# Optimization experiments

Hardware: AMD Instinct MI355X
Metric: run time of the kernel (lower is better)

## Reference

```python
import jax, jax.numpy as jnp
import numpy as np

# ---- hyperparameters (from args defaults) ----
TEMPERATURE = 0.07
ALPHA = 0.5
OT_EPSILON = 0.1
OT_ITERS = 20
HOLO_WEIGHT = 1.0
RKD_DISTANCE_WEIGHT = 1.0
RKD_ANGLE_WEIGHT = 2.0
GLOBAL_RKD_WEIGHT = 10.0
MATRYOSHKA_DIMS = [128, 768]
MATRYOSHKA_WEIGHTS = [1.0, 2.0]

B, N, H_S, H_T, D_REP = 64, 256, 768, 1024, 768


def l2norm(x, axis=-1):
    # F.normalize(p=2): x / max(||x||, eps)
    n = jnp.sqrt(jnp.sum(x * x, axis=axis, keepdims=True))
    return x / jnp.maximum(n, 1e-12)


def pairwise_distance(x):
    # [n, d] -> [n, n] squared-euclidean-style distances
    sq = jnp.sum(x * x, axis=1, keepdims=True)
    return sq + sq.T - 2.0 * (x @ x.T)


def huber(diff):
    a = jnp.abs(diff)
    return jnp.where(a < 1.0, 0.5 * a * a, a - 0.5)


def rkd_distance_loss(s, t):
    n = s.shape[0]
    mask = jnp.triu(jnp.ones((n, n), dtype=bool), k=1)
    cnt = jnp.sum(mask.astype(s.dtype))
    ds, dt = pairwise_distance(s), pairwise_distance(t)
    mean_s = jax.lax.stop_gradient(jnp.sum(jnp.where(mask, ds, 0.0)) / cnt) + 1e-8
    mean_t = jax.lax.stop_gradient(jnp.sum(jnp.where(mask, dt, 0.0)) / cnt) + 1e-8
    loss = huber(ds / mean_s - dt / mean_t)
    return jnp.sum(jnp.where(mask, loss, 0.0)) / cnt


def angle_potentials(x):
    # diffs[i, j] = x[j] - x[i]
    diffs = x[None, :, :] - x[:, None, :]
    e = diffs / (jnp.linalg.norm(diffs, axis=-1, keepdims=True) + 1e-8)
    return jnp.einsum('ijd,kjd->ijk', e, e)


def rkd_angle_loss(s, t):
    psi_s, psi_t = angle_potentials(s), angle_potentials(t)
    n = psi_s.shape[0]
    idx = jnp.arange(n)
    i, j, k = idx[:, None, None], idx[None, :, None], idx[None, None, :]
    mask = (i != j) & (i != k) & (j != k)  # exclude degenerate triplets
    cnt = jnp.sum(mask.astype(s.dtype))
    loss = huber(psi_s - psi_t)
    return jnp.sum(jnp.where(mask, loss, 0.0)) / cnt


def saliency_measure(h, temp=1.0):
    # softmax over token axis of hidden-state norms -> [B, N, 1]
    norms = jnp.linalg.norm(h, axis=-1)
    return jax.nn.softmax(norms / temp, axis=-1)[..., None]


def structure_matrix(z):
    zn = l2norm(z, axis=-1)
    return 1.0 - jnp.einsum('bnd,bmd->bnm', zn, zn)


def sinkhorn_knopp_log_domain(C, mu, nu):
    # C: [B, Ns, Nt]; mu: [B, Ns, 1]; nu: [B, Nt, 1]
    log_K = -C / OT_EPSILON
    log_mu = jnp.log(mu + 1e-8)
    log_nu = jnp.log(nu + 1e-8)
    u = jnp.zeros_like(mu)
    v = jnp.zeros_like(nu)
    for _ in range(OT_ITERS):
        u = log_mu - jax.scipy.special.logsumexp(
            log_K + jnp.swapaxes(v, 1, 2), axis=2, keepdims=True)
        v = log_nu - jax.scipy.special.logsumexp(
            jnp.swapaxes(log_K, 1, 2) + jnp.swapaxes(u, 1, 2),
            axis=2, keepdims=True)
    return jnp.exp(u + log_K + jnp.swapaxes(v, 1, 2))


def fused_gromov_wasserstein(z_s, z_t, proj_w, proj_b):
    mu = saliency_measure(z_s)   # [B, N, 1]
    nu = saliency_measure(z_t)   # [B, N, 1]
    C_s = structure_matrix(z_s)  # [B, N, N]
    C_t = structure_matrix(z_t)
    z_s_norm = l2norm(z_s @ proj_w + proj_b, axis=-1)
    z_t_norm = l2norm(z_t, axis=-1)
    M = 1.0 - jnp.einsum('bnd,bmd->bnm', z_s_norm, z_t_norm)
    Gamma = sinkhorn_knopp_log_domain(M, mu, nu)
    feat_loss = jnp.mean(jnp.sum(M * Gamma, axis=(1, 2)))
    Gamma_norm = Gamma / (jnp.sum(Gamma, axis=2, keepdims=True) + 1e-8)
    C_t_mapped = jnp.einsum('bnm,bmk,blk->bnl', Gamma_norm, C_t, Gamma_norm)
    w = jnp.einsum('bni,bmi->bnm', mu, mu)  # mu @ mu^T
    struct_loss = jnp.mean(jnp.sum((C_s - C_t_mapped) ** 2 * w, axis=(1, 2)))
    return (1.0 - ALPHA) * feat_loss + ALPHA * struct_loss


def cross_entropy_inbatch(scores):
    # labels = arange(B)
    logZ = jax.scipy.special.logsumexp(scores, axis=1)
    return jnp.mean(logZ - jnp.diagonal(scores))


def setup_inputs() -> dict:
    key = jax.random.key(0)
    ks = jax.random.split(key, 10)
    return {
        's_q_reps': jax.random.normal(ks[0], (B, D_REP), jnp.float32),
        's_p_reps': jax.random.normal(ks[1], (B, D_REP), jnp.float32),
        't_q_reps': jax.random.normal(ks[2], (B, D_REP), jnp.float32),
        't_p_reps': jax.random.normal(ks[3], (B, D_REP), jnp.float32),
        's_q_states': jax.random.normal(ks[4], (B, N, H_S), jnp.float32),
        's_p_states': jax.random.normal(ks[5], (B, N, H_S), jnp.float32),
        't_q_states': jax.random.normal(ks[6], (B, N, H_T), jnp.float32),
        't_p_states': jax.random.normal(ks[7], (B, N, H_T), jnp.float32),
        'proj_w': jax.random.normal(ks[8], (H_S, H_T), jnp.float32) * (H_S ** -0.5),
        'proj_b': jnp.zeros((H_T,), jnp.float32),
    }


def reference(s_q_reps, s_p_reps, t_q_reps, t_p_reps,
              s_q_states, s_p_states, t_q_states, t_p_states,
              proj_w, proj_b):
    # teacher outputs are computed under torch.no_grad()
    t_q_reps = jax.lax.stop_gradient(t_q_reps)
    t_p_reps = jax.lax.stop_gradient(t_p_reps)
    t_q_states = jax.lax.stop_gradient(t_q_states)
    t_p_states = jax.lax.stop_gradient(t_p_states)

    contrastive_acc = 0.0
    holo_acc = 0.0
    rkd_acc = 0.0
    for dim, dim_weight in zip(MATRYOSHKA_DIMS, MATRYOSHKA_WEIGHTS):
        s_q_slice = l2norm(s_q_reps[:, :dim])
        s_p_slice = l2norm(s_p_reps[:, :dim])
        scores = (s_q_slice @ s_p_slice.T) / TEMPERATURE
        contrastive_acc += dim_weight * cross_entropy_inbatch(scores)
        if dim <= 128:
            s_batch = jnp.concatenate([s_q_slice, s_p_slice], axis=0)
            t_batch = jnp.concatenate(
                [l2norm(t_q_reps[:, :dim]), l2norm(t_p_reps[:, :dim])], axis=0)
            loss_dist = rkd_distance_loss(s_batch, t_batch)
            loss_angle = rkd_angle_loss(s_batch, t_batch)
            rkd_val = (RKD_DISTANCE_WEIGHT * loss_dist
                       + RKD_ANGLE_WEIGHT * loss_angle)
            rkd_acc += GLOBAL_RKD_WEIGHT * rkd_val * 2.0
        else:
            loss_q = fused_gromov_wasserstein(s_q_states, t_q_states, proj_w, proj_b)
            loss_p = fused_gromov_wasserstein(s_p_states, t_p_states, proj_w, proj_b)
            holo_acc += HOLO_WEIGHT * 0.5 * (loss_q + loss_p)
    return contrastive_acc + holo_acc + rkd_acc
```

## Files before the change

### kernel.cpp

```cpp
#include <hip/hip_runtime.h>
#include <math.h>

#define NB   64
#define NN   256
#define HSS  768
#define HTT  1024
#define ROWS (NB*NN)
#define C2LOG 14.426950408889634f

typedef unsigned short u16;
typedef __attribute__((ext_vector_type(8))) short bf16x8;
typedef __attribute__((ext_vector_type(4))) float f32x4;

#define LIDX(r,c) (((r)<<8) + (((((c)>>3) + (r)) & 31)<<3) + ((c)&7))
#define EIDX(r,c) (((r)<<7) + (((((c)>>3) + (r)) & 15)<<3) + ((c)&7))

__device__ __forceinline__ void gl16(const u16* g, u16* l){
  __builtin_amdgcn_global_load_lds(
      (const __attribute__((address_space(1))) unsigned int*)g,
      (__attribute__((address_space(3))) unsigned int*)l,
      16, 0, 0);
}

static const size_t OFF_ACC   = 0;
static const size_t OFF_SQ128 = 16;
static const size_t OFF_SP128 = OFF_SQ128 + 64*128;
static const size_t OFF_TQ128 = OFF_SP128 + 64*128;
static const size_t OFF_TP128 = OFF_TQ128 + 64*128;
static const size_t OFF_SQ768 = OFF_TP128 + 64*128;
static const size_t OFF_SP768 = OFF_SQ768 + 64*768;
static const size_t OFF_DS    = OFF_SP768 + 64*768;
static const size_t OFF_DT    = OFF_DS + 128*128;
static const size_t OFF_CS    = OFF_DT + 128*128;
static const size_t OFF_MBF   = OFF_CS  + (size_t)2*NB*NN*NN;
static const size_t OFF_ZS_BF = OFF_MBF + (size_t)NB*NN*NN;
static const size_t OFF_ZT_BF = OFF_ZS_BF + (size_t)ROWS*HSS/2;
static const size_t OFF_WT_BF = OFF_ZT_BF + (size_t)ROWS*HTT/2;
static const size_t OFF_ZSP_BF= OFF_WT_BF + (size_t)HTT*HSS/2;
static const size_t OFF_GN_BF = OFF_ZSP_BF+ (size_t)ROWS*HTT/2;
static const size_t OFF_CT_BF = OFF_GN_BF + (size_t)NB*NN*NN;
static const size_t OFF_T_BF  = OFF_ZS_BF;
static const size_t OFF_NS    = OFF_CT_BF + (size_t)NB*NN*NN;
static const size_t OFF_NT    = OFF_NS + ROWS;
static const size_t OFF_NSP   = OFF_NT + ROWS;
static const size_t OFF_MU    = OFF_NSP + ROWS;
static const size_t OFF_NU    = OFF_MU + 2*ROWS;


__device__ __forceinline__ float wred_sum(float v){
  #pragma unroll
  for(int o=32;o>0;o>>=1) v += __shfl_xor(v,o,64);
  return v;
}
__device__ __forceinline__ float wred_max(float v){
  #pragma unroll
  for(int o=32;o>0;o>>=1) v = fmaxf(v, __shfl_xor(v,o,64));
  return v;
}
__device__ __forceinline__ u16 f2bf(float f){
  unsigned u = __float_as_uint(f);
  unsigned r = (u + 0x7fffu + ((u>>16)&1u)) >> 16;
  return (u16)r;
}
__device__ __forceinline__ float bf2f(u16 h){
  return __uint_as_float(((unsigned)h)<<16);
}
__device__ __forceinline__ float rdlane(float v, int srcLane){
  return __uint_as_float(__builtin_amdgcn_readlane(__float_as_uint(v), srcLane));
}

__global__ __launch_bounds__(256) void k_l2norm_all(
    const float* __restrict__ sq, const float* __restrict__ sp,
    const float* __restrict__ tq, const float* __restrict__ tp,
    float* __restrict__ ws){
  int bid = blockIdx.x;
  int r = bid & 63;
  const float* in; float* out; int kuse;
  if(bid < 64)       { in = sq; out = ws + OFF_SQ128; kuse = 128; }
  else if(bid < 128) { in = sp; out = ws + OFF_SP128; kuse = 128; }
  else if(bid < 192) { in = tq; out = ws + OFF_TQ128; kuse = 128; }
  else if(bid < 256) { in = tp; out = ws + OFF_TP128; kuse = 128; }
  else if(bid < 320) { in = sq; out = ws + OFF_SQ768; kuse = 768; }
  else               { in = sp; out = ws + OFF_SP768; kuse = 768; }
  const float* row = in + (size_t)r*768;
  float ss = 0.f;
  for(int d=threadIdx.x; d<kuse; d+=256){ float x=row[d]; ss += x*x; }
  ss = wred_sum(ss);
  __shared__ float sm[4];
  if((threadIdx.x&63)==0) sm[threadIdx.x>>6]=ss;
  __syncthreads();
  float tot = sm[0]+sm[1]+sm[2]+sm[3];
  float inv = 1.f / fmaxf(sqrtf(tot), 1e-12f);
  for(int d=threadIdx.x; d<kuse; d+=256) out[(size_t)r*kuse + d] = row[d]*inv;
}

__global__ __launch_bounds__(512) void k_contrastive2(const float* __restrict__ ws,
    float* __restrict__ acc){
  int bid = blockIdx.x;
  int i = bid & 63;
  int big = bid >> 6;
  const float* q = ws + (big ? OFF_SQ768 : OFF_SQ128);
  const float* p = ws + (big ? OFF_SP768 : OFF_SP128);
  int dim = big ? 768 : 128;
  float weight = big ? 2.f : 1.f;
  int j = threadIdx.x & 63;
  int part = threadIdx.x >> 6;
  const float* qi = q + (size_t)i*dim;
  const float* pj = p + (size_t)j*dim;
  int seg = dim >> 3;
  int d0 = part*seg;
  float dot = 0.f;
  for(int d=d0; d<d0+seg; d+=4){
    float4 a = *(const float4*)(qi+d);
    float4 b = *(const float4*)(pj+d);
    dot = fmaf(a.x,b.x,dot);
    dot = fmaf(a.y,b.y,dot);
    dot = fmaf(a.z,b.z,dot);
    dot = fmaf(a.w,b.w,dot);
  }
  __shared__ float sm[8][64];
  sm[part][j] = dot;
  __syncthreads();
  if(part==0){
    float s = 0.f;
    #pragma unroll
    for(int k=0;k<8;k++) s += sm[k][j];
    s = s / 0.07f;
    float mx = wred_max(s);
    float e = expf(s - mx);
    float Z = wred_sum(e);
    float logZ = mx + logf(Z);
    float diag = __shfl(s, i, 64);
    if(j==0) atomicAdd(acc+0, weight*(logZ - diag)*(1.f/64.f));
  }
}

__global__ __launch_bounds__(128) void k_gram_ds(const float* __restrict__ sb,
    const float* __restrict__ tb, float* __restrict__ ds, float* __restrict__ dt,
    float* __restrict__ acc){
  int r = blockIdx.x, c = threadIdx.x;
  const float* sr = sb + r*128; const float* sc = sb + c*128;
  const float* tr = tb + r*128; const float* tc = tb + c*128;
  float dot_s=0,ssr=0,ssc=0,dot_t=0,tsr=0,tsc=0;
  for(int d=0; d<128; d++){
    float a=sr[d], b=sc[d]; dot_s += a*b; ssr += a*a; ssc += b*b;
    float at=tr[d], bt=tc[d]; dot_t += at*bt; tsr += at*at; tsc += bt*bt;
  }
  float dv = ssr + ssc - 2.f*dot_s;
  float tv = tsr + tsc - 2.f*dot_t;
  ds[r*128+c] = dv; dt[r*128+c] = tv;
  float ms = (c>r)? dv : 0.f;
  float mt = (c>r)? tv : 0.f;
  ms = wred_sum(ms); mt = wred_sum(mt);
  __shared__ float sm[2][2];
  if((threadIdx.x&63)==0){ sm[0][threadIdx.x>>6]=ms; sm[1][threadIdx.x>>6]=mt; }
  __syncthreads();
  if(threadIdx.x==0){ atomicAdd(acc+1, sm[0][0]+sm[0][1]); atomicAdd(acc+2, sm[1][0]+sm[1][1]); }
}

__global__ __launch_bounds__(128) void k_rkd_dist(const float* __restrict__ ds,
    const float* __restrict__ dt, float* __restrict__ acc){
  int r=blockIdx.x, c=threadIdx.x;
  float mean_s = acc[1]*(1.f/8128.f) + 1e-8f;
  float mean_t = acc[2]*(1.f/8128.f) + 1e-8f;
  float h=0.f;
  if(c>r){
    float diff = ds[r*128+c]/mean_s - dt[r*128+c]/mean_t;
    float a = fabsf(diff);
    h = (a<1.f)? 0.5f*a*a : a-0.5f;
  }
  h = wred_sum(h);
  __shared__ float sm[2];
  if((threadIdx.x&63)==0) sm[threadIdx.x>>6]=h;
  __syncthreads();
  if(threadIdx.x==0) atomicAdd(acc+3, sm[0]+sm[1]);
}

#define RKD_LDS 65536
__global__ __launch_bounds__(256, 1) void k_rkd_angle_mfma(
    const float* __restrict__ sb, const float* __restrict__ tb,
    float* __restrict__ accp)
{
  extern __shared__ u16 eSh[];
  u16* Es = eSh;
  u16* Et = eSh + 128*128;
  const int j    = blockIdx.x >> 1;
  const int half = blockIdx.x & 1;
  const int tid = threadIdx.x;
  {
    const int i = tid >> 1, h = tid & 1;
    #pragma unroll
    for(int which=0; which<2; which++){
      const float* xb = which ? tb : sb;
      u16* E = which ? Et : Es;
      const float* xj = xb + j*128 + h*64;
      const float* xi = xb + i*128 + h*64;
      float ss = 0.f;
      #pragma unroll
      for(int d4=0; d4<16; d4++){
        float4 a = *(const float4*)(xj + d4*4);
        float4 b = *(const float4*)(xi + d4*4);
        float d0=a.x-b.x, d1=a.y-b.y, d2=a.z-b.z, d3=a.w-b.w;
        ss += d0*d0+d1*d1+d2*d2+d3*d3;
      }
      ss += __shfl_xor(ss, 1, 64);
      float inv = (i==j) ? 0.f : 1.f/(sqrtf(ss)+1e-8f);
      #pragma unroll
      for(int d4=0; d4<16; d4++){
        float4 a = *(const float4*)(xj + d4*4);
        float4 b = *(const float4*)(xi + d4*4);
        int c = h*64 + d4*4;
        E[EIDX(i,c+0)] = f2bf((a.x-b.x)*inv);
        E[EIDX(i,c+1)] = f2bf((a.y-b.y)*inv);
        E[EIDX(i,c+2)] = f2bf((a.z-b.z)*inv);
        E[EIDX(i,c+3)] = f2bf((a.w-b.w)*inv);
      }
    }
  }
  __syncthreads();
  const int w = tid >> 6, lane = tid & 63;
  const int q = lane >> 4, loc = lane & 15;
  float hsum = 0.f;
  #pragma unroll
  for(int ni=0; ni<4; ni++){
    const int cb = half*64 + ni*16;
    #pragma unroll
    for(int mi=0; mi<2; mi++){
      const int rb = w*32 + mi*16;
      f32x4 as_ = {0.f,0.f,0.f,0.f}, at_ = {0.f,0.f,0.f,0.f};
      #pragma unroll
      for(int k0=0; k0<128; k0+=32){
        int ra = rb + loc, rbn = cb + loc;
        int ca = k0 + q*8;
        bf16x8 aS = *(const bf16x8*)(Es + EIDX(ra, ca));
        bf16x8 bS = *(const bf16x8*)(Es + EIDX(rbn, ca));
        bf16x8 aT = *(const bf16x8*)(Et + EIDX(ra, ca));
        bf16x8 bT = *(const bf16x8*)(Et + EIDX(rbn, ca));
        as_ = __builtin_amdgcn_mfma_f32_16x16x32_bf16(aS, bS, as_, 0,0,0);
        at_ = __builtin_amdgcn_mfma_f32_16x16x32_bf16(aT, bT, at_, 0,0,0);
      }
      #pragma unroll
      for(int jj=0; jj<4; jj++){
        int row = rb + q*4 + jj, col = cb + loc;
        if(row != col){
          float d = as_[jj] - at_[jj];
          float a = fabsf(d);
          hsum += (a < 1.f) ? 0.5f*a*a : a - 0.5f;
        }
      }
    }
  }
  hsum = wred_sum(hsum);
  __syncthreads();
  float* red = (float*)eSh;
  if(lane==0) red[w] = hsum;
  __syncthreads();
  if(tid==0) atomicAdd(accp+4, red[0]+red[1]+red[2]+red[3]);
}

__global__ __launch_bounds__(256) void k_cvt_norm(const float* __restrict__ in,
    u16* __restrict__ out, float* __restrict__ nrm, int K){
  int w = threadIdx.x >> 6, l = threadIdx.x & 63;
  int r = blockIdx.x*4 + w;
  const float* row = in + (size_t)r*K;
  u16* orow = out + (size_t)r*K;
  float ss = 0.f;
  int nv = K >> 8;
  for(int i=0;i<nv;i++){
    int d = l*4 + i*256;
    float4 x = *(const float4*)(row + d);
    ushort4 o; o.x=f2bf(x.x); o.y=f2bf(x.y); o.z=f2bf(x.z); o.w=f2bf(x.w);
    *(ushort4*)(orow + d) = o;
    ss += x.x*x.x + x.y*x.y + x.z*x.z + x.w*x.w;
  }
  ss = wred_sum(ss);
  if(l==0) nrm[r] = sqrtf(ss);
}

__global__ __launch_bounds__(256) void k_row_norm_bf16(const u16* __restrict__ z,
    float* __restrict__ nrm, int K){
  int w = threadIdx.x >> 6, l = threadIdx.x & 63;
  int r = blockIdx.x*4 + w;
  const u16* row = z + (size_t)r*K;
  float ss = 0.f;
  int nv = K >> 9;
  for(int i=0;i<nv;i++){
    int d = l*8 + i*512;
    uint4 v = *(const uint4*)(row + d);
    float a0=__uint_as_float(v.x<<16), a1=__uint_as_float(v.x&0xffff0000u);
    float a2=__uint_as_float(v.y<<16), a3=__uint_as_float(v.y&0xffff0000u);
    float a4=__uint_as_float(v.z<<16), a5=__uint_as_float(v.z&0xffff0000u);
    float a6=__uint_as_float(v.w<<16), a7=__uint_as_float(v.w&0xffff0000u);
    ss += a0*a0+a1*a1+a2*a2+a3*a3+a4*a4+a5*a5+a6*a6+a7*a7;
  }
  ss = wred_sum(ss);
  if(l==0) nrm[r] = sqrtf(ss);
}

__global__ void k_wt(const float* __restrict__ W, u16* __restrict__ Wt){
  __shared__ float t[32][33];
  int k0 = blockIdx.y*32, n0 = blockIdx.x*32;
  int tx = threadIdx.x, ty = threadIdx.y;
  for(int r=0;r<32;r+=8) t[ty+r][tx] = W[(size_t)(k0+ty+r)*HTT + n0+tx];
  __syncthreads();
  for(int r=0;r<32;r+=8) Wt[(size_t)(n0+ty+r)*HSS + k0+tx] = f2bf(t[tx][ty+r]);
}

__global__ __launch_bounds__(256) void k_saliency2(const float* __restrict__ ns,
    const float* __restrict__ nt, float* __restrict__ omu, float* __restrict__ onu){
  int b0 = blockIdx.x, n = threadIdx.x;
  const float* nrm = (b0 < NB) ? ns : nt;
  float* out = (b0 < NB) ? omu : onu;
  int b = b0 & 63;
  float x = nrm[b*NN+n];
  float mx = wred_max(x);
  __shared__ float sm[4], sm2[4];
  if((n&63)==0) sm[n>>6]=mx;
  __syncthreads();
  mx = fmaxf(fmaxf(sm[0],sm[1]),fmaxf(sm[2],sm[3]));
  float e = expf(x-mx);
  float s = wred_sum(e);
  if((n&63)==0) sm2[n>>6]=s;
  __syncthreads();
  s = sm2[0]+sm2[1]+sm2[2]+sm2[3];
  out[b*NN+n] = e/s;
}

enum { MODE_PROJ=0, MODE_COST=1, MODE_PLAIN=2, MODE_STRUCT=3 };

template<int MODE>
__global__ __launch_bounds__(256) void k_mfma(
    const u16* __restrict__ A, int lda, long bA,
    const u16* __restrict__ B, int ldb, long bB,
    int K,
    float* __restrict__ outF, u16* __restrict__ outB, int ldo, long bO,
    const float* __restrict__ nx, const float* __restrict__ ny,
    const float* __restrict__ bias,
    const float* __restrict__ Cs, const float* __restrict__ mu,
    float* __restrict__ accp)
{
  __shared__ u16 As[128*32];
  __shared__ u16 Bs[128*32];
  __shared__ float red[4];

  int gx = gridDim.x, gy = gridDim.y;
  int flat = blockIdx.x + gx*(blockIdx.y + gy*blockIdx.z);
  int nwg  = gx*gy*gridDim.z;
  int cpx  = nwg >> 3;
  int lg   = (flat & 7)*cpx + (flat >> 3);
  int bx   = lg % gx;
  int rest = lg / gx;
  int by   = rest % gy;
  int b    = rest / gy;

  const u16* Ab = A + (size_t)b*bA;
  const u16* Bb = B + (size_t)b*bB;
  int tid = threadIdx.x;
  int lane = tid & 63, w = tid >> 6;
  int m0 = by*128, n0 = bx*128;
  int row_off = (w>>1)*64, col_off = (w&1)*64;
  int q = lane>>4, loc = lane&15;
  f32x4 acc[4][4] = {};

  const int srow = (lane >> 2);
  const int sslot = lane & 3;

  for(int k0=0;k0<K;k0+=32){
    #pragma unroll
    for(int h=0;h<2;h++){
      int row = h*64 + w*16 + srow;
      int ca  = (sslot ^ ((row>>1)&3))*8;
      u16* ldst = As + h*2048 + w*512 + lane*8;
      u16* ldstB= Bs + h*2048 + w*512 + lane*8;
      gl16(Ab + (size_t)(m0+row)*lda + k0 + ca, ldst);
      gl16(Bb + (size_t)(n0+row)*ldb + k0 + ca, ldstB);
    }
    __syncthreads();
    bf16x8 af[4], bfr[4];
    #pragma unroll
    for(int mi=0;mi<4;mi++){
      int r = row_off + mi*16 + loc;
      int slot = q ^ ((r>>1)&3);
      af[mi] = *(const bf16x8*)(As + r*32 + slot*8);
    }
    #pragma unroll
    for(int ni=0;ni<4;ni++){
      int r = col_off + ni*16 + loc;
      int slot = q ^ ((r>>1)&3);
      bfr[ni] = *(const bf16x8*)(Bs + r*32 + slot*8);
    }
    #pragma unroll
    for(int mi=0;mi<4;mi++)
      #pragma unroll
      for(int ni=0;ni<4;ni++)
        acc[mi][ni] = __builtin_amdgcn_mfma_f32_16x16x32_bf16(af[mi], bfr[ni], acc[mi][ni], 0,0,0);
    __syncthreads();
  }

  float* outFb = outF ? outF + (size_t)b*bO : nullptr;
  u16*   outBb = outB ? outB + (size_t)b*bO : nullptr;
  const float* nxb = nx ? nx + (size_t)b*NN : nullptr;
  const float* nyb = ny ? ny + (size_t)b*NN : nullptr;
  const float* Cb  = (MODE==MODE_STRUCT) ? Cs + (size_t)b*bO : nullptr;
  const float* mb  = (MODE==MODE_STRUCT) ? mu + (size_t)b*NN : nullptr;
  float lsum = 0.f;
  #pragma unroll
  for(int mi=0;mi<4;mi++){
    #pragma unroll
    for(int j=0;j<4;j++){
      int row = m0 + row_off + mi*16 + q*4 + j;
      float ir = 0.f, mr = 0.f;
      if(MODE==MODE_COST)   ir = 1.f/fmaxf(nxb[row],1e-12f);
      if(MODE==MODE_STRUCT) mr = mb[row];
      #pragma unroll
      for(int ni=0;ni<4;ni++){
        int col = n0 + col_off + ni*16 + loc;
        float v = acc[mi][ni][j];
        if(MODE==MODE_PROJ){
          v += bias[col];
          outBb[(size_t)row*ldo + col] = f2bf(v);
        } else if(MODE==MODE_COST){
          float ic = 1.f/fmaxf(nyb[col],1e-12f);
          v = 1.f - v*ir*ic;
          if(outFb) outFb[(size_t)row*ldo + col] = v;
          if(outBb) outBb[(size_t)row*ldo + col] = f2bf(v);
        } else if(MODE==MODE_PLAIN){
          outBb[(size_t)row*ldo + col] = f2bf(v);
        } else {
          float d = Cb[(size_t)row*ldo + col] - v;
          lsum += d*d*mr*mb[col];
        }
      }
    }
  }
  if(MODE==MODE_STRUCT){
    lsum = wred_sum(lsum);
    if(lane==0) red[w] = lsum;
    __syncthreads();
    if(tid==0) atomicAdd(accp+6, red[0]+red[1]+red[2]+red[3]);
  }
}

#define SINK_DYN_LDS 131072
__global__ __launch_bounds__(1024, 1) void k_sinkhorn_fused(
    const u16* __restrict__ Mbf, const float* __restrict__ muL,
    const float* __restrict__ nuL, u16* __restrict__ Gn, float* __restrict__ accp)
{
  extern __shared__ u16 Ks[];
  __shared__ __align__(16) float partA[1024];
  __shared__ __align__(16) float partB[4096];
  __shared__ __align__(16) float svw[1024];
  __shared__ __align__(16) float smu_s[256], snu_s[256], sv_ep[256];
  __shared__ float red[16];

  const int b = blockIdx.x;
  const int t = threadIdx.x;
  const u16* Mb = Mbf + (size_t)b*NN*NN;

  #pragma unroll
  for(int i=0;i<16;i++){
    int e = (i*1024 + t)*4;
    int r = e>>8, c = e&255;
    ushort4 mv = *(const ushort4*)(Mb + e);
    ushort4 o;
    o.x = f2bf(exp2f(-C2LOG*bf2f(mv.x)));
    o.y = f2bf(exp2f(-C2LOG*bf2f(mv.y)));
    o.z = f2bf(exp2f(-C2LOG*bf2f(mv.z)));
    o.w = f2bf(exp2f(-C2LOG*bf2f(mv.w)));
    *(ushort4*)(Ks + LIDX(r,c)) = o;
  }
  if(t < NN){
    smu_s[t] = muL[(size_t)b*NN+t] + 1e-8f;
    snu_s[t] = nuL[(size_t)b*NN+t] + 1e-8f;
  }
  __syncthreads();

  const int w = t>>6, l = t&63;
  const int r_ = t & 255, p_ = t >> 8;
  const int rw = (w<<4) + (l&15);
  const int cl = (p_<<6) + l;
  float* svslot = svw + (w<<6);

  uint4 kreg[8];
  #pragma unroll
  for(int jj=0;jj<8;jj++)
    kreg[jj] = *(const uint4*)(Ks + LIDX(r_, (p_<<6)+(jj<<3)));

  #pragma unroll 1
  for(int it=0; it<21; it++){
    float vl;
    if(it==0){ vl = 1.f; }
    else {
      float t0=0.f,t1=0.f,t2=0.f,t3=0.f;
      #pragma unroll
      for(int ww=0; ww<4; ww++){
        t0 += partB[((ww*4+0)<<8) + cl];
        t1 += partB[((ww*4+1)<<8) + cl];
        t2 += partB[((ww*4+2)<<8) + cl];
        t3 += partB[((ww*4+3)<<8) + cl];
      }
      vl = snu_s[cl] / ((t0+t1)+(t2+t3));
    }
    svslot[l] = vl;
    if(it==20 && (w&3)==0) sv_ep[cl] = vl;
    float s0=0.f, s1=0.f, s2=0.f, s3=0.f;
    #pragma unroll
    for(int jj=0;jj<8;jj++){
      uint4 kv = kreg[jj];
      float4 va = *(const float4*)(svslot + (jj<<3));
      float4 vb = *(const float4*)(svslot + (jj<<3) + 4);
      s0 = fmaf(__uint_as_float(kv.x<<16),           va.x, s0);
      s1 = fmaf(__uint_as_float(kv.x & 0xffff0000u), va.y, s1);
      s2 = fmaf(__uint_as_float(kv.y<<16),           va.z, s2);
      s3 = fmaf(__uint_as_float(kv.y & 0xffff0000u), va.w, s3);
      s0 = fmaf(__uint_as_float(kv.z<<16),           vb.x, s0);
      s1 = fmaf(__uint_as_float(kv.z & 0xffff0000u), vb.y, s1);
      s2 = fmaf(__uint_as_float(kv.w<<16),           vb.z, s2);
      s3 = fmaf(__uint_as_float(kv.w & 0xffff0000u), vb.w, s3);
    }
    float sacc = (s0+s1)+(s2+s3);
    if(it==20) svw[t] = sacc;
    else       partA[t] = sacc;
    __syncthreads();
    if(it==20) break;

    float S = (partA[rw] + partA[256+rw]) + (partA[512+rw] + partA[768+rw]);
    float ul = smu_s[rw] / S;
    float cs0=0.f,cs1=0.f,cs2=0.f,cs3=0.f;
    #pragma unroll
    for(int rr=0; rr<16; rr++){
      float ur = rdlane(ul, rr);
      ushort4 kv = *(const ushort4*)(Ks + LIDX((w<<4)+rr, l<<2));
      cs0 = fmaf(bf2f(kv.x), ur, cs0);
      cs1 = fmaf(bf2f(kv.y), ur, cs1);
      cs2 = fmaf(bf2f(kv.z), ur, cs2);
      cs3 = fmaf(bf2f(kv.w), ur, cs3);
    }
    float4 o; o.x=cs0; o.y=cs1; o.z=cs2; o.w=cs3;
    *(float4*)(partB + (w<<8) + (l<<2)) = o;
    __syncthreads();
  }

  float Sold = (partA[rw] + partA[256+rw]) + (partA[512+rw] + partA[768+rw]);
  float ul   = smu_s[rw] / Sold;
  float Snew = (svw[rw] + svw[256+rw]) + (svw[512+rw] + svw[768+rw]);
  float invl = 1.f / (ul*Snew + 1e-8f);

  u16* Gb = Gn + (size_t)b*NN*NN;
  const float IC = -1.f/C2LOG;
  float4 v4 = *(const float4*)(sv_ep + (l<<2));
  float fl = 0.f;
  #pragma unroll
  for(int rr=0; rr<16; rr++){
    int r = (w<<4) + rr;
    float ur  = rdlane(ul, rr);
    float inv = rdlane(invl, rr);
    ushort4 kv = *(const ushort4*)(Ks + LIDX(r, l<<2));
    float k0=bf2f(kv.x), k1=bf2f(kv.y), k2=bf2f(kv.z), k3=bf2f(kv.w);
    float g0=ur*k0*v4.x, g1=ur*k1*v4.y, g2=ur*k2*v4.z, g3=ur*k3*v4.w;
    fl += g0*(__log2f(k0)*IC) + g1*(__log2f(k1)*IC)
        + g2*(__log2f(k2)*IC) + g3*(__log2f(k3)*IC);
    ushort4 o;
    o.x=f2bf(g0*inv); o.y=f2bf(g1*inv); o.z=f2bf(g2*inv); o.w=f2bf(g3*inv);
    *(ushort4*)(Gb + (size_t)r*NN + (l<<2)) = o;
  }
  fl = wred_sum(fl);
  if(l==0) red[w] = fl;
  __syncthreads();
  if(t==0){
    float s=0.f;
    #pragma unroll
    for(int i=0;i<16;i++) s+=red[i];
    atomicAdd(accp+5, s);
  }
}

__global__ void k_final(const float* __restrict__ acc, float* __restrict__ out){
  out[0] = acc[0]
         + 20.f*acc[3]*(1.f/8128.f)
         + 40.f*acc[4]*(1.f/2048256.f)
         + 0.25f*(acc[5]+acc[6])*(1.f/64.f);
}

extern "C" void kernel_launch(void* const* d_in, const int* in_sizes, int n_in,
                              void* d_out, int out_size, void* d_ws, size_t ws_size,
                              hipStream_t stream) {
  const float* s_q_reps   = (const float*)d_in[0];
  const float* s_p_reps   = (const float*)d_in[1];
  const float* t_q_reps   = (const float*)d_in[2];
  const float* t_p_reps   = (const float*)d_in[3];
  const float* s_q_states = (const float*)d_in[4];
  const float* s_p_states = (const float*)d_in[5];
  const float* t_q_states = (const float*)d_in[6];
  const float* t_p_states = (const float*)d_in[7];
  const float* proj_w     = (const float*)d_in[8];
  const float* proj_b     = (const float*)d_in[9];
  float* ws = (float*)d_ws;
  float* acc = ws + OFF_ACC;
  u16* M_BF   = (u16*)(ws + OFF_MBF);
  u16* ZS_BF  = (u16*)(ws + OFF_ZS_BF);
  u16* ZT_BF  = (u16*)(ws + OFF_ZT_BF);
  u16* WT_BF  = (u16*)(ws + OFF_WT_BF);
  u16* ZSP_BF = (u16*)(ws + OFF_ZSP_BF);
  u16* GN_BF  = (u16*)(ws + OFF_GN_BF);
  u16* CT_BF  = (u16*)(ws + OFF_CT_BF);
  u16* T_BF   = (u16*)(ws + OFF_T_BF);

  hipFuncSetAttribute(reinterpret_cast<const void*>(k_sinkhorn_fused),
                      hipFuncAttributeMaxDynamicSharedMemorySize, SINK_DYN_LDS);
  hipFuncSetAttribute(reinterpret_cast<const void*>(k_rkd_angle_mfma),
                      hipFuncAttributeMaxDynamicSharedMemorySize, RKD_LDS);

  hipMemsetAsync(acc, 0, 16*sizeof(float), stream);

  k_l2norm_all<<<384,256,0,stream>>>(s_q_reps, s_p_reps, t_q_reps, t_p_reps, ws);
  k_contrastive2<<<128,512,0,stream>>>(ws, acc);
  k_gram_ds<<<128,128,0,stream>>>(ws+OFF_SQ128, ws+OFF_TQ128, ws+OFF_DS, ws+OFF_DT, acc);
  k_rkd_dist<<<128,128,0,stream>>>(ws+OFF_DS, ws+OFF_DT, acc);
  k_rkd_angle_mfma<<<256,256,RKD_LDS,stream>>>(ws+OFF_SQ128, ws+OFF_TQ128, acc);

  k_wt<<<dim3(HTT/32, HSS/32),dim3(32,8),0,stream>>>(proj_w, WT_BF);

  for(int pass=0; pass<2; pass++){
    const float* zs = pass ? s_p_states : s_q_states;
    const float* zt = pass ? t_p_states : t_q_states;
    size_t po  = (size_t)pass*NB*NN*NN;
    size_t pr  = (size_t)pass*ROWS;
    k_cvt_norm<<<ROWS/4,256,0,stream>>>(zs, ZS_BF, ws+OFF_NS, HSS);
    k_cvt_norm<<<ROWS/4,256,0,stream>>>(zt, ZT_BF, ws+OFF_NT, HTT);
    k_saliency2<<<128,256,0,stream>>>(ws+OFF_NS, ws+OFF_NT, ws+OFF_MU+pr, ws+OFF_NU+pr);
    k_mfma<MODE_PROJ><<<dim3(HTT/128, ROWS/128, 1),256,0,stream>>>(
        ZS_BF, HSS, 0, WT_BF, HSS, 0, HSS,
        nullptr, ZSP_BF, HTT, 0,
        nullptr, nullptr, proj_b, nullptr, nullptr, nullptr);
    k_row_norm_bf16<<<ROWS/4,256,0,stream>>>(ZSP_BF, ws+OFF_NSP, HTT);
    k_mfma<MODE_COST><<<dim3(2,2,NB),256,0,stream>>>(
        ZS_BF, HSS, (long)NN*HSS, ZS_BF, HSS, (long)NN*HSS, HSS,
        ws+OFF_CS+po, nullptr, NN, (long)NN*NN,
        ws+OFF_NS, ws+OFF_NS, nullptr, nullptr, nullptr, nullptr);
    k_mfma<MODE_COST><<<dim3(2,2,NB),256,0,stream>>>(
        ZT_BF, HTT, (long)NN*HTT, ZT_BF, HTT, (long)NN*HTT, HTT,
        nullptr, CT_BF+po, NN, (long)NN*NN,
        ws+OFF_NT, ws+OFF_NT, nullptr, nullptr, nullptr, nullptr);
    k_mfma<MODE_COST><<<dim3(2,2,NB),256,0,stream>>>(
        ZSP_BF, HTT, (long)NN*HTT, ZT_BF, HTT, (long)NN*HTT, HTT,
        nullptr, M_BF+po, NN, (long)NN*NN,
        ws+OFF_NSP, ws+OFF_NT, nullptr, nullptr, nullptr, nullptr);
  }

  k_sinkhorn_fused<<<2*NB,1024,SINK_DYN_LDS,stream>>>(
      M_BF, ws+OFF_MU, ws+OFF_NU, GN_BF, acc);

  k_mfma<MODE_PLAIN><<<dim3(2,2,2*NB),256,0,stream>>>(
      GN_BF, NN, (long)NN*NN, CT_BF, NN, (long)NN*NN, NN,
      nullptr, T_BF, NN, (long)NN*NN,
      nullptr, nullptr, nullptr, nullptr, nullptr, nullptr);
  k_mfma<MODE_STRUCT><<<dim3(2,2,2*NB),256,0,stream>>>(
      T_BF, NN, (long)NN*NN, GN_BF, NN, (long)NN*NN, NN,
      nullptr, nullptr, NN, (long)NN*NN,
      nullptr, nullptr, nullptr, ws+OFF_CS, ws+OFF_MU, acc);

  k_final<<<1,1,0,stream>>>(acc, (float*)d_out);
}
```

Measured before the change: 680.0 us.

## Restructure Sinkhorn loop to stream K from LDS and use shuffle reductions

The fused Sinkhorn kernel no longer caches a row slice of K in registers. Each iteration now reads K from LDS for the row-sum matvec. Row and column partial sums are reduced with wave shuffles instead of separate LDS partial buffers, and u, v and the final inverse are kept in shared arrays. The column-normalisation step becomes its own phase with an extra barrier per iteration. This cuts register pressure and LDS footprint, but adds LDS traffic for K and one more __syncthreads per iteration.

```diff
diff --git a/kernel.cpp b/kernel.cpp
--- a/kernel.cpp
+++ b/kernel.cpp
@@ -64,9 +64,6 @@
 }
 __device__ __forceinline__ float bf2f(u16 h){
   return __uint_as_float(((unsigned)h)<<16);
-}
-__device__ __forceinline__ float rdlane(float v, int srcLane){
-  return __uint_as_float(__builtin_amdgcn_readlane(__float_as_uint(v), srcLane));
 }
 
 __global__ __launch_bounds__(256) void k_l2norm_all(
@@ -447,10 +444,8 @@
     const float* __restrict__ nuL, u16* __restrict__ Gn, float* __restrict__ accp)
 {
   extern __shared__ u16 Ks[];
-  __shared__ __align__(16) float partA[1024];
   __shared__ __align__(16) float partB[4096];
-  __shared__ __align__(16) float svw[1024];
-  __shared__ __align__(16) float smu_s[256], snu_s[256], sv_ep[256];
+  __shared__ __align__(16) float su[256], sv[256], smu_s[256], snu_s[256], sinv[256];
   __shared__ float red[16];
 
   const int b = blockIdx.x;
@@ -472,43 +467,23 @@
   if(t < NN){
     smu_s[t] = muL[(size_t)b*NN+t] + 1e-8f;
     snu_s[t] = nuL[(size_t)b*NN+t] + 1e-8f;
+    sv[t] = 1.f;
   }
   __syncthreads();
 
   const int w = t>>6, l = t&63;
-  const int r_ = t & 255, p_ = t >> 8;
-  const int rw = (w<<4) + (l&15);
-  const int cl = (p_<<6) + l;
-  float* svslot = svw + (w<<6);
-
-  uint4 kreg[8];
-  #pragma unroll
-  for(int jj=0;jj<8;jj++)
-    kreg[jj] = *(const uint4*)(Ks + LIDX(r_, (p_<<6)+(jj<<3)));
+  const int ra = (w<<4) + (l&15);
+  const int qa = l>>4;
 
   #pragma unroll 1
-  for(int it=0; it<21; it++){
-    float vl;
-    if(it==0){ vl = 1.f; }
-    else {
-      float t0=0.f,t1=0.f,t2=0.f,t3=0.f;
-      #pragma unroll
-      for(int ww=0; ww<4; ww++){
-        t0 += partB[((ww*4+0)<<8) + cl];
-        t1 += partB[((ww*4+1)<<8) + cl];
-        t2 += partB[((ww*4+2)<<8) + cl];
-        t3 += partB[((ww*4+3)<<8) + cl];
-      }
-      vl = snu_s[cl] / ((t0+t1)+(t2+t3));
-    }
-    svslot[l] = vl;
-    if(it==20 && (w&3)==0) sv_ep[cl] = vl;
+  for(int it=0; it<=20; ++it){
     float s0=0.f, s1=0.f, s2=0.f, s3=0.f;
     #pragma unroll
     for(int jj=0;jj<8;jj++){
-      uint4 kv = kreg[jj];
-      float4 va = *(const float4*)(svslot + (jj<<3));
-      float4 vb = *(const float4*)(svslot + (jj<<3) + 4);
+      int c0 = (qa<<6) + (jj<<3);
+      uint4 kv = *(const uint4*)(Ks + LIDX(ra, c0));
+      float4 va = *(const float4*)(sv + c0);
+      float4 vb = *(const float4*)(sv + c0 + 4);
       s0 = fmaf(__uint_as_float(kv.x<<16),           va.x, s0);
       s1 = fmaf(__uint_as_float(kv.x & 0xffff0000u), va.y, s1);
       s2 = fmaf(__uint_as_float(kv.y<<16),           va.z, s2);
@@ -518,19 +493,22 @@
       s2 = fmaf(__uint_as_float(kv.w<<16),           vb.z, s2);
       s3 = fmaf(__uint_as_float(kv.w & 0xffff0000u), vb.w, s3);
     }
-    float sacc = (s0+s1)+(s2+s3);
-    if(it==20) svw[t] = sacc;
-    else       partA[t] = sacc;
+    float S = (s0+s1)+(s2+s3);
+    S += __shfl_xor(S, 16, 64);
+    S += __shfl_xor(S, 32, 64);
+    if(qa==0){
+      if(it<20) su[ra]   = smu_s[ra] / S;
+      else      sinv[ra] = 1.f / (su[ra]*S + 1e-8f);
+    }
     __syncthreads();
     if(it==20) break;
 
-    float S = (partA[rw] + partA[256+rw]) + (partA[512+rw] + partA[768+rw]);
-    float ul = smu_s[rw] / S;
     float cs0=0.f,cs1=0.f,cs2=0.f,cs3=0.f;
     #pragma unroll
     for(int rr=0; rr<16; rr++){
-      float ur = rdlane(ul, rr);
-      ushort4 kv = *(const ushort4*)(Ks + LIDX((w<<4)+rr, l<<2));
+      int r = (w<<4) + rr;
+      ushort4 kv = *(const ushort4*)(Ks + LIDX(r, l<<2));
+      float ur = su[r];
       cs0 = fmaf(bf2f(kv.x), ur, cs0);
       cs1 = fmaf(bf2f(kv.y), ur, cs1);
       cs2 = fmaf(bf2f(kv.z), ur, cs2);
@@ -539,22 +517,27 @@
     float4 o; o.x=cs0; o.y=cs1; o.z=cs2; o.w=cs3;
     *(float4*)(partB + (w<<8) + (l<<2)) = o;
     __syncthreads();
-  }
-
-  float Sold = (partA[rw] + partA[256+rw]) + (partA[512+rw] + partA[768+rw]);
-  float ul   = smu_s[rw] / Sold;
-  float Snew = (svw[rw] + svw[256+rw]) + (svw[512+rw] + svw[768+rw]);
-  float invl = 1.f / (ul*Snew + 1e-8f);
+
+    {
+      int c = t>>2, g = t&3;
+      float T = partB[((g*4+0)<<8)+c] + partB[((g*4+1)<<8)+c]
+              + partB[((g*4+2)<<8)+c] + partB[((g*4+3)<<8)+c];
+      T += __shfl_xor(T, 1, 64);
+      T += __shfl_xor(T, 2, 64);
+      if(g==0) sv[c] = snu_s[c] / T;
+    }
+    __syncthreads();
+  }
 
   u16* Gb = Gn + (size_t)b*NN*NN;
   const float IC = -1.f/C2LOG;
-  float4 v4 = *(const float4*)(sv_ep + (l<<2));
+  float4 v4 = *(const float4*)(sv + (l<<2));
   float fl = 0.f;
   #pragma unroll
   for(int rr=0; rr<16; rr++){
     int r = (w<<4) + rr;
-    float ur  = rdlane(ul, rr);
-    float inv = rdlane(invl, rr);
+    float ur  = su[r];
+    float inv = sinv[r];
     ushort4 kv = *(const ushort4*)(Ks + LIDX(r, l<<2));
     float k0=bf2f(kv.x), k1=bf2f(kv.y), k2=bf2f(kv.z), k3=bf2f(kv.w);
     float g0=ur*k0*v4.x, g1=ur*k1*v4.y, g2=ur*k2*v4.z, g3=ur*k3*v4.w;
```

Measured after the change: 686.9 us. Within noise of the previous version (+1.0%).
